# Performance work log

Measured on AMD Instinct MI355X. Metric: run time of the kernel, lower is better.

Reference implementation:

```python
import jax, jax.numpy as jnp
import numpy as np

N = 32768   # nodes
E = 524288  # edges (avg degree 16)
F = 32      # num_features
H = 512     # hidden_channels
C = 10      # num_classes
G = 64      # graphs in batch


def setup_inputs() -> dict:
    key = jax.random.key(0)
    ks = jax.random.split(key, 16)
    s = 0.05  # weight init scale
    f32 = jnp.float32
    return {
        "x": jax.random.normal(ks[0], (N, F), f32),
        "edge_index": jax.random.randint(ks[1], (2, E), 0, N),
        "batch_index": jnp.sort(jax.random.randint(ks[2], (N,), 0, G)),
        # initial_conv: F -> H  (PyG GraphConv: lin_root on x, lin_rel on aggregated neighbors)
        "w_root0": jax.random.normal(ks[3], (F, H), f32) * s,
        "w_rel0": jax.random.normal(ks[4], (F, H), f32) * s,
        "b0": jnp.zeros((H,), f32),
        # conv1..conv4 stacked: H -> H
        "w_root": jax.random.normal(ks[5], (4, H, H), f32) * s,
        "w_rel": jax.random.normal(ks[6], (4, H, H), f32) * s,
        "b": jnp.zeros((4, H), f32),
        # MLP tail
        "lin1_w": jax.random.normal(ks[7], (2 * H, H), f32) * s,
        "lin1_b": jnp.zeros((H,), f32),
        "lin2_w": jax.random.normal(ks[8], (H, H), f32) * s,
        "lin2_b": jnp.zeros((H,), f32),
        "lin3_w": jax.random.normal(ks[9], (H, C), f32) * s,
        "lin3_b": jnp.zeros((C,), f32),
    }


def _graph_conv(h, src, dst, w_root, w_rel, bias):
    # out_i = h_i @ W_root + (sum_{j->i} h_j) @ W_rel + b   (PyG GraphConv, aggr='add')
    agg = jax.ops.segment_sum(h[src], dst, num_segments=N)
    return h @ w_root + agg @ w_rel + bias


def reference(x, edge_index, batch_index,
              w_root0, w_rel0, b0, w_root, w_rel, b,
              lin1_w, lin1_b, lin2_w, lin2_b, lin3_w, lin3_b):
    src, dst = edge_index[0], edge_index[1]
    h = jnp.tanh(_graph_conv(x, src, dst, w_root0, w_rel0, b0))
    for i in range(4):  # fixed small layer loop
        h = jnp.tanh(_graph_conv(h, src, dst, w_root[i], w_rel[i], b[i]))
    # global max + mean pool over graphs
    gmax = jax.ops.segment_max(h, batch_index, num_segments=G)
    gsum = jax.ops.segment_sum(h, batch_index, num_segments=G)
    cnt = jax.ops.segment_sum(jnp.ones((N,), h.dtype), batch_index, num_segments=G)
    gmean = gsum / jnp.maximum(cnt, 1.0)[:, None]
    g = jnp.concatenate([gmax, gmean], axis=1)  # [G, 2H]
    # dropout is identity at inference (training=False)
    g = jnp.tanh(g @ lin1_w + lin1_b)
    g = jnp.tanh(g @ lin2_w + lin2_b)
    logits = g @ lin3_w + lin3_b
    return jax.nn.log_softmax(logits, axis=1)
```

## Files before the change

### kernel.cpp

```cpp
#include <hip/hip_runtime.h>
#include <hip/hip_bf16.h>
#include <math.h>

#define NN 32768
#define EE 524288
#define FF 32
#define HH 512
#define GG 64
#define CC 10

typedef __attribute__((ext_vector_type(8))) short short8;
typedef __attribute__((ext_vector_type(4))) float floatx4;

__device__ __forceinline__ float bf16_to_f32(unsigned short u) {
    union { unsigned int u; float f; } v;
    v.u = ((unsigned int)u) << 16;
    return v.f;
}
__device__ __forceinline__ unsigned short f32_to_bf16(float f) {
    union { float f; unsigned int u; } v;
    v.f = f;
    unsigned int u = v.u;
    u += 0x7FFFu + ((u >> 16) & 1u);
    return (unsigned short)(u >> 16);
}
__device__ __forceinline__ float fast_tanh(float x) {
    float e = __expf(2.0f * x);
    return 1.0f - 2.0f * __builtin_amdgcn_rcpf(e + 1.0f);
}

__global__ void prep_wt0_kernel(const float* __restrict__ wr, const float* __restrict__ wl,
                                unsigned short* __restrict__ WT0) {
    int t = blockIdx.x * blockDim.x + threadIdx.x;
    if (t >= 512 * 64) return;
    int n = t >> 6, k = t & 63;
    float v = (k < 32) ? wr[k * 512 + n] : wl[(k - 32) * 512 + n];
    WT0[t] = f32_to_bf16(v);
}

__global__ void prep_wt_kernel(const float* __restrict__ wroot, const float* __restrict__ wrel,
                               unsigned short* __restrict__ WT) {
    int t = blockIdx.x * blockDim.x + threadIdx.x;
    int l = t >> 19;
    int r = t & 524287;
    int n = r >> 10, k = r & 1023;
    float v = (k < 512) ? wroot[(size_t)l * 262144 + k * 512 + n]
                        : wrel[(size_t)l * 262144 + (k - 512) * 512 + n];
    WT[t] = f32_to_bf16(v);
}

__global__ void build_x0_kernel(const float* __restrict__ x, unsigned short* __restrict__ X0) {
    int t = blockIdx.x * blockDim.x + threadIdx.x;
    if (t >= NN * 32) return;
    int i = t >> 5, c = t & 31;
    X0[(size_t)i * 64 + c] = f32_to_bf16(x[t]);
}

__global__ void zero_i32(int* __restrict__ p, int n) {
    int i = blockIdx.x * blockDim.x + threadIdx.x;
    if (i < n) p[i] = 0;
}
__global__ void hist_kernel(const int* __restrict__ dst, int* __restrict__ counts) {
    int e = blockIdx.x * blockDim.x + threadIdx.x;
    if (e < EE) atomicAdd(&counts[dst[e]], 1);
}
__global__ __launch_bounds__(1024) void scan_kernel(const int* __restrict__ counts,
                                                    int* __restrict__ rowStart,
                                                    int* __restrict__ cursor) {
    __shared__ int part[1024];
    const int t = threadIdx.x;
    const int base = t * 32;
    int local[32];
    const int4* cp = (const int4*)(counts + base);
    int s = 0;
#pragma unroll
    for (int ii = 0; ii < 8; ++ii) {
        int4 v = cp[ii];
        local[ii * 4 + 0] = v.x; local[ii * 4 + 1] = v.y;
        local[ii * 4 + 2] = v.z; local[ii * 4 + 3] = v.w;
        s += v.x + v.y + v.z + v.w;
    }
    part[t] = s;
    __syncthreads();
    for (int off = 1; off < 1024; off <<= 1) {
        int v = (t >= off) ? part[t - off] : 0;
        __syncthreads();
        part[t] += v;
        __syncthreads();
    }
    int run = part[t] - s;
#pragma unroll
    for (int i = 0; i < 32; ++i) {
        rowStart[base + i] = run;
        cursor[base + i] = run;
        run += local[i];
    }
    if (t == 1023) rowStart[NN] = run;
}
__global__ void scatter_kernel(const int* __restrict__ src, const int* __restrict__ dst,
                               int* __restrict__ cursor, int* __restrict__ ssrc) {
    int e = blockIdx.x * blockDim.x + threadIdx.x;
    if (e < EE) {
        int p = atomicAdd(&cursor[dst[e]], 1);
        ssrc[p] = src[e];
    }
}

__device__ __forceinline__ void acc8(float* a, uint4 d) {
    a[0] += bf16_to_f32((unsigned short)(d.x & 0xFFFFu));
    a[1] += bf16_to_f32((unsigned short)(d.x >> 16));
    a[2] += bf16_to_f32((unsigned short)(d.y & 0xFFFFu));
    a[3] += bf16_to_f32((unsigned short)(d.y >> 16));
    a[4] += bf16_to_f32((unsigned short)(d.z & 0xFFFFu));
    a[5] += bf16_to_f32((unsigned short)(d.z >> 16));
    a[6] += bf16_to_f32((unsigned short)(d.w & 0xFFFFu));
    a[7] += bf16_to_f32((unsigned short)(d.w >> 16));
}

__global__ __launch_bounds__(256) void agg_kernel(const unsigned short* __restrict__ Xh, int ldh,
                                                  int cols, unsigned short* __restrict__ Xagg,
                                                  int ldagg, const int* __restrict__ rowStart,
                                                  const int* __restrict__ ssrc) {
    const int node = blockIdx.x * 4 + (threadIdx.x >> 6);
    const int lane = threadIdx.x & 63;
    const int chunks = cols >> 3;
    if (node >= NN || lane >= chunks) return;
    const int s = rowStart[node];
    const int e = rowStart[node + 1];
    float a[8] = {0.f, 0.f, 0.f, 0.f, 0.f, 0.f, 0.f, 0.f};
    const unsigned short* base = Xh + lane * 8;
    int i = s;
    for (; i + 4 <= e; i += 4) {
        int j0 = ssrc[i], j1 = ssrc[i + 1], j2 = ssrc[i + 2], j3 = ssrc[i + 3];
        uint4 d0 = *(const uint4*)(base + (size_t)j0 * ldh);
        uint4 d1 = *(const uint4*)(base + (size_t)j1 * ldh);
        uint4 d2 = *(const uint4*)(base + (size_t)j2 * ldh);
        uint4 d3 = *(const uint4*)(base + (size_t)j3 * ldh);
        acc8(a, d0); acc8(a, d1); acc8(a, d2); acc8(a, d3);
    }
    for (; i < e; ++i) {
        int j = ssrc[i];
        uint4 d = *(const uint4*)(base + (size_t)j * ldh);
        acc8(a, d);
    }
    unsigned short* out = Xagg + (size_t)node * ldagg + lane * 8;
#pragma unroll
    for (int c = 0; c < 8; ++c) out[c] = f32_to_bf16(a[c]);
}

__global__ __launch_bounds__(256) void agg_slice_kernel(const unsigned short* __restrict__ Xh,
                                                        unsigned short* __restrict__ Xagg,
                                                        const int* __restrict__ rowStart,
                                                        const int* __restrict__ ssrc) {
    const int slice = blockIdx.x & 7;
    const int nb = blockIdx.x >> 3;
    const int wv = threadIdx.x >> 6;
    const int lane = threadIdx.x & 63;
    const int ln = lane >> 3;
    const int lc = lane & 7;
    const int node = nb * 32 + wv * 8 + ln;
    const int colOff = slice * 64 + lc * 8;
    const int s = rowStart[node];
    const int e = rowStart[node + 1];
    float a[8] = {0.f, 0.f, 0.f, 0.f, 0.f, 0.f, 0.f, 0.f};
    const unsigned short* base = Xh + colOff;
    int i = s;
    for (; i + 4 <= e; i += 4) {
        int j0 = ssrc[i], j1 = ssrc[i + 1], j2 = ssrc[i + 2], j3 = ssrc[i + 3];
        uint4 d0 = *(const uint4*)(base + (size_t)j0 * 1024);
        uint4 d1 = *(const uint4*)(base + (size_t)j1 * 1024);
        uint4 d2 = *(const uint4*)(base + (size_t)j2 * 1024);
        uint4 d3 = *(const uint4*)(base + (size_t)j3 * 1024);
        acc8(a, d0); acc8(a, d1); acc8(a, d2); acc8(a, d3);
    }
    for (; i < e; ++i) {
        int j = ssrc[i];
        uint4 d = *(const uint4*)(base + (size_t)j * 1024);
        acc8(a, d);
    }
    unsigned short* out = Xagg + (size_t)node * 1024 + colOff;
#pragma unroll
    for (int c = 0; c < 8; ++c) out[c] = f32_to_bf16(a[c]);
}

__global__ __launch_bounds__(256) void gemm_bias_tanh(const unsigned short* __restrict__ Xin,
                                                      int ldin, int K,
                                                      const unsigned short* __restrict__ WT,
                                                      const float* __restrict__ bias,
                                                      unsigned short* __restrict__ Xout,
                                                      int ldout) {
    __shared__ __align__(16) unsigned short As[128 * 32];
    __shared__ __align__(16) unsigned short Bs[128 * 32];
    const int tid = threadIdx.x;
    const int lane = tid & 63;
    const int wave = tid >> 6;
    const int wm = wave >> 1, wn = wave & 1;
    const int bm = blockIdx.x, bn = blockIdx.y;

    floatx4 acc[4][4] = {};

    const int lrow = lane >> 2;
    const int lcol = (lane & 3) << 3;
    const unsigned short* Abase = Xin + (size_t)(bm * 128) * ldin;
    const unsigned short* Bbase = WT + (size_t)(bn * 128) * K;
    const int m = lane & 15;
    const int quad = lane >> 4;

    for (int k0 = 0; k0 < K; k0 += 32) {
        __syncthreads();
#pragma unroll
        for (int q = 0; q < 2; ++q) {
            const int rr = wave * 32 + q * 16;
            const unsigned short* sa = Abase + (size_t)(rr + lrow) * ldin + (k0 + lcol);
            const unsigned short* sb = Bbase + (size_t)(rr + lrow) * K + (k0 + lcol);
            __builtin_amdgcn_global_load_lds(
                (const __attribute__((address_space(1))) void*)sa,
                (__attribute__((address_space(3))) void*)(&As[rr * 32]), 16, 0, 0);
            __builtin_amdgcn_global_load_lds(
                (const __attribute__((address_space(1))) void*)sb,
                (__attribute__((address_space(3))) void*)(&Bs[rr * 32]), 16, 0, 0);
        }
        __syncthreads();
        short8 af[4], bfr[4];
#pragma unroll
        for (int t = 0; t < 4; ++t)
            af[t] = *(const short8*)&As[(wm * 64 + t * 16 + m) * 32 + quad * 8];
#pragma unroll
        for (int t = 0; t < 4; ++t)
            bfr[t] = *(const short8*)&Bs[(wn * 64 + t * 16 + m) * 32 + quad * 8];
#pragma unroll
        for (int mt = 0; mt < 4; ++mt)
#pragma unroll
            for (int nt = 0; nt < 4; ++nt)
                acc[mt][nt] =
                    __builtin_amdgcn_mfma_f32_16x16x32_bf16(af[mt], bfr[nt], acc[mt][nt], 0, 0, 0);
    }

    const int row0 = bm * 128 + wm * 64;
    const int col0 = bn * 128 + wn * 64;
#pragma unroll
    for (int mt = 0; mt < 4; ++mt) {
#pragma unroll
        for (int nt = 0; nt < 4; ++nt) {
            const int col = col0 + nt * 16 + m;
            const float bv = bias[col];
#pragma unroll
            for (int r = 0; r < 4; ++r) {
                const int row = row0 + mt * 16 + quad * 4 + r;
                float v = fast_tanh(acc[mt][nt][r] + bv);
                Xout[(size_t)row * ldout + col] = f32_to_bf16(v);
            }
        }
    }
}

__global__ __launch_bounds__(256) void pool_partial(const unsigned short* __restrict__ h,
                                                    const int* __restrict__ batch,
                                                    float* __restrict__ part) {
    const int gi = blockIdx.x, rs = blockIdx.y, t = threadIdx.x;
    int lo = 0, hi = NN;
    while (lo < hi) { int mid = (lo + hi) >> 1; if (batch[mid] < gi) lo = mid + 1; else hi = mid; }
    const int start = lo;
    hi = NN;
    while (lo < hi) { int mid = (lo + hi) >> 1; if (batch[mid] < gi + 1) lo = mid + 1; else hi = mid; }
    const int end = lo;
    const int len = end - start;
    const int q = (len + 3) >> 2;
    int r0 = start + rs * q;
    int r1 = r0 + q; if (r1 > end) r1 = end; if (r0 > end) r0 = end;
    float mx0 = -INFINITY, mx1 = -INFINITY, s0 = 0.f, s1 = 0.f;
    int i = r0;
    for (; i + 2 <= r1; i += 2) {
        unsigned int d0 = *(const unsigned int*)(h + (size_t)i * 1024 + t * 2);
        unsigned int d1 = *(const unsigned int*)(h + (size_t)(i + 1) * 1024 + t * 2);
        float v0 = bf16_to_f32((unsigned short)(d0 & 0xFFFFu));
        float v1 = bf16_to_f32((unsigned short)(d0 >> 16));
        float w0 = bf16_to_f32((unsigned short)(d1 & 0xFFFFu));
        float w1 = bf16_to_f32((unsigned short)(d1 >> 16));
        mx0 = fmaxf(mx0, fmaxf(v0, w0)); mx1 = fmaxf(mx1, fmaxf(v1, w1));
        s0 += v0 + w0; s1 += v1 + w1;
    }
    for (; i < r1; ++i) {
        unsigned int d0 = *(const unsigned int*)(h + (size_t)i * 1024 + t * 2);
        float v0 = bf16_to_f32((unsigned short)(d0 & 0xFFFFu));
        float v1 = bf16_to_f32((unsigned short)(d0 >> 16));
        mx0 = fmaxf(mx0, v0); mx1 = fmaxf(mx1, v1);
        s0 += v0; s1 += v1;
    }
    float* p = part + ((size_t)gi * 4 + rs) * 1024;
    p[t * 2] = mx0; p[t * 2 + 1] = mx1;
    p[512 + t * 2] = s0; p[512 + t * 2 + 1] = s1;
}

__global__ __launch_bounds__(256) void pool_combine(const float* __restrict__ part,
                                                    const int* __restrict__ batch,
                                                    float* __restrict__ gT) {
    const int gi = blockIdx.x, t = threadIdx.x;
    int lo = 0, hi = NN;
    while (lo < hi) { int mid = (lo + hi) >> 1; if (batch[mid] < gi) lo = mid + 1; else hi = mid; }
    const int start = lo;
    hi = NN;
    while (lo < hi) { int mid = (lo + hi) >> 1; if (batch[mid] < gi + 1) lo = mid + 1; else hi = mid; }
    int cnt = lo - start; if (cnt < 1) cnt = 1;
    const float inv = 1.0f / (float)cnt;
    float mx0 = -INFINITY, mx1 = -INFINITY, s0 = 0.f, s1 = 0.f;
#pragma unroll
    for (int rs = 0; rs < 4; ++rs) {
        const float* p = part + ((size_t)gi * 4 + rs) * 1024;
        mx0 = fmaxf(mx0, p[t * 2]); mx1 = fmaxf(mx1, p[t * 2 + 1]);
        s0 += p[512 + t * 2]; s1 += p[512 + t * 2 + 1];
    }
    gT[(size_t)(2 * t) * 64 + gi]        = mx0;
    gT[(size_t)(2 * t + 1) * 64 + gi]    = mx1;
    gT[(size_t)(512 + 2 * t) * 64 + gi]  = s0 * inv;
    gT[(size_t)(512 + 2 * t + 1) * 64 + gi] = s1 * inv;
}

__global__ __launch_bounds__(256) void mlp_splitk(const float* __restrict__ ginT,
                                                  const float* __restrict__ W,
                                                  int Ndim,
                                                  float* __restrict__ partial) {
    __shared__ float gsT[64][68];
    __shared__ float Ws[64][68];
    const int t = threadIdx.x;
    const int wv = t >> 6, l = t & 63;
    const int nb = blockIdx.x, kb = blockIdx.y;
    const int n0 = nb * 64;
    const int gr = t >> 2;
    const int c4 = (t & 3) * 16;
    float acc[16] = {};
#pragma unroll
    for (int sub = 0; sub < 2; ++sub) {
        const int k0 = kb * 128 + sub * 64;
        __syncthreads();
        {
            const float4* gsrc = (const float4*)(ginT + (size_t)(k0 + gr) * 64 + c4);
            float4* gd = (float4*)&gsT[gr][c4];
            gd[0] = gsrc[0]; gd[1] = gsrc[1]; gd[2] = gsrc[2]; gd[3] = gsrc[3];
            const float4* wsrc = (const float4*)(W + (size_t)(k0 + gr) * Ndim + n0 + c4);
            float4* wd = (float4*)&Ws[gr][c4];
            wd[0] = wsrc[0]; wd[1] = wsrc[1]; wd[2] = wsrc[2]; wd[3] = wsrc[3];
        }
        __syncthreads();
#pragma unroll 4
        for (int kk = 0; kk < 64; ++kk) {
            const float wval = Ws[kk][l];
            const float4* gv = (const float4*)&gsT[kk][wv * 16];
            float4 g0 = gv[0], g1 = gv[1], g2 = gv[2], g3 = gv[3];
            acc[0]  = fmaf(g0.x, wval, acc[0]);  acc[1]  = fmaf(g0.y, wval, acc[1]);
            acc[2]  = fmaf(g0.z, wval, acc[2]);  acc[3]  = fmaf(g0.w, wval, acc[3]);
            acc[4]  = fmaf(g1.x, wval, acc[4]);  acc[5]  = fmaf(g1.y, wval, acc[5]);
            acc[6]  = fmaf(g1.z, wval, acc[6]);  acc[7]  = fmaf(g1.w, wval, acc[7]);
            acc[8]  = fmaf(g2.x, wval, acc[8]);  acc[9]  = fmaf(g2.y, wval, acc[9]);
            acc[10] = fmaf(g2.z, wval, acc[10]); acc[11] = fmaf(g2.w, wval, acc[11]);
            acc[12] = fmaf(g3.x, wval, acc[12]); acc[13] = fmaf(g3.y, wval, acc[13]);
            acc[14] = fmaf(g3.z, wval, acc[14]); acc[15] = fmaf(g3.w, wval, acc[15]);
        }
    }
    float* p = partial + ((size_t)kb * 64) * Ndim;
#pragma unroll
    for (int g = 0; g < 16; ++g)
        p[(size_t)(wv * 16 + g) * Ndim + n0 + l] = acc[g];
}

__global__ __launch_bounds__(256) void mlp_combine(const float* __restrict__ partial, int nparts,
                                                   const float* __restrict__ bias, int Ndim,
                                                   float* __restrict__ outN,
                                                   float* __restrict__ outT) {
    const int idx = blockIdx.x * 256 + threadIdx.x;
    if (idx >= 64 * Ndim) return;
    const int g = idx / Ndim, n = idx - g * Ndim;
    float s = bias[n];
    for (int kb = 0; kb < nparts; ++kb)
        s += partial[((size_t)kb * 64 + g) * Ndim + n];
    const float v = fast_tanh(s);
    if (outN) outN[(size_t)g * Ndim + n] = v;
    if (outT) outT[(size_t)n * 64 + g] = v;
}

__global__ __launch_bounds__(64) void head_kernel(const float* __restrict__ g2,
                                                  const float* __restrict__ W,
                                                  const float* __restrict__ b,
                                                  float* __restrict__ out) {
    const int gi = blockIdx.x, t = threadIdx.x;
    const float4* gp = (const float4*)(g2 + (size_t)gi * HH + t * 8);
    float4 ga = gp[0], gb = gp[1];
    float gv[8] = {ga.x, ga.y, ga.z, ga.w, gb.x, gb.y, gb.z, gb.w};
    float logits[CC];
#pragma unroll
    for (int c = 0; c < CC; ++c) {
        float p = 0.f;
#pragma unroll
        for (int j = 0; j < 8; ++j)
            p = fmaf(gv[j], W[(t * 8 + j) * CC + c], p);
#pragma unroll
        for (int off = 32; off > 0; off >>= 1)
            p += __shfl_xor(p, off, 64);
        logits[c] = p + b[c];
    }
    if (t == 0) {
        float mx = logits[0];
#pragma unroll
        for (int c = 1; c < CC; ++c) mx = fmaxf(mx, logits[c]);
        float s = 0.f;
#pragma unroll
        for (int c = 0; c < CC; ++c) s += expf(logits[c] - mx);
        float lse = mx + logf(s);
#pragma unroll
        for (int c = 0; c < CC; ++c) out[(size_t)gi * CC + c] = logits[c] - lse;
    }
}

extern "C" void kernel_launch(void* const* d_in, const int* in_sizes, int n_in,
                              void* d_out, int out_size, void* d_ws, size_t ws_size,
                              hipStream_t stream) {
    const float* x       = (const float*)d_in[0];
    const int*   ei      = (const int*)d_in[1];
    const int*   batch   = (const int*)d_in[2];
    const float* w_root0 = (const float*)d_in[3];
    const float* w_rel0  = (const float*)d_in[4];
    const float* b0      = (const float*)d_in[5];
    const float* w_root  = (const float*)d_in[6];
    const float* w_rel   = (const float*)d_in[7];
    const float* bvec    = (const float*)d_in[8];
    const float* lin1_w  = (const float*)d_in[9];
    const float* lin1_b  = (const float*)d_in[10];
    const float* lin2_w  = (const float*)d_in[11];
    const float* lin2_b  = (const float*)d_in[12];
    const float* lin3_w  = (const float*)d_in[13];
    const float* lin3_b  = (const float*)d_in[14];
    float* out = (float*)d_out;

    char* w = (char*)d_ws;
    size_t off = 0;
    auto alloc = [&](size_t bytes) -> char* {
        char* p = w + off;
        off += (bytes + 255) & ~(size_t)255;
        return p;
    };
    unsigned short* Xa  = (unsigned short*)alloc((size_t)NN * 1024 * 2);
    unsigned short* Xb  = (unsigned short*)alloc((size_t)NN * 1024 * 2);
    unsigned short* X0  = (unsigned short*)alloc((size_t)NN * 64 * 2);
    unsigned short* WT0 = (unsigned short*)alloc(512 * 64 * 2);
    unsigned short* WTs = (unsigned short*)alloc((size_t)4 * 512 * 1024 * 2);
    int* counts   = (int*)alloc((size_t)NN * 4);
    int* rowStart = (int*)alloc((size_t)(NN + 1) * 4);
    int* cursor   = (int*)alloc((size_t)NN * 4);
    int* ssrc     = (int*)alloc((size_t)EE * 4);
    float* gbufT  = (float*)alloc((size_t)1024 * 64 * 4);
    float* g1T    = (float*)alloc((size_t)512 * 64 * 4);
    float* g2buf  = (float*)alloc((size_t)GG * 512 * 4);
    float* mlpPart = (float*)alloc((size_t)8 * 64 * 512 * 4);
    float* part   = (float*)X0;

    const int* esrc = ei;
    const int* edst = ei + EE;

    prep_wt0_kernel<<<128, 256, 0, stream>>>(w_root0, w_rel0, WT0);
    prep_wt_kernel<<<8192, 256, 0, stream>>>(w_root, w_rel, WTs);
    build_x0_kernel<<<4096, 256, 0, stream>>>(x, X0);

    zero_i32<<<128, 256, 0, stream>>>(counts, NN);
    hist_kernel<<<2048, 256, 0, stream>>>(edst, counts);
    scan_kernel<<<1, 1024, 0, stream>>>(counts, rowStart, cursor);
    scatter_kernel<<<2048, 256, 0, stream>>>(esrc, edst, cursor, ssrc);

    agg_kernel<<<8192, 256, 0, stream>>>(X0, 64, 32, X0 + 32, 64, rowStart, ssrc);
    gemm_bias_tanh<<<dim3(256, 4), 256, 0, stream>>>(X0, 64, 64, WT0, b0, Xa, 1024);

    agg_slice_kernel<<<8192, 256, 0, stream>>>(Xa, Xa + 512, rowStart, ssrc);
    gemm_bias_tanh<<<dim3(256, 4), 256, 0, stream>>>(Xa, 1024, 1024, WTs + 0 * 524288, bvec + 0, Xb, 1024);
    agg_slice_kernel<<<8192, 256, 0, stream>>>(Xb, Xb + 512, rowStart, ssrc);
    gemm_bias_tanh<<<dim3(256, 4), 256, 0, stream>>>(Xb, 1024, 1024, WTs + 1 * 524288, bvec + 512, Xa, 1024);
    agg_slice_kernel<<<8192, 256, 0, stream>>>(Xa, Xa + 512, rowStart, ssrc);
    gemm_bias_tanh<<<dim3(256, 4), 256, 0, stream>>>(Xa, 1024, 1024, WTs + 2 * 524288, bvec + 1024, Xb, 1024);
    agg_slice_kernel<<<8192, 256, 0, stream>>>(Xb, Xb + 512, rowStart, ssrc);
    gemm_bias_tanh<<<dim3(256, 4), 256, 0, stream>>>(Xb, 1024, 1024, WTs + 3 * 524288, bvec + 1536, Xa, 1024);

    pool_partial<<<dim3(GG, 4), 256, 0, stream>>>(Xa, batch, part);
    pool_combine<<<GG, 256, 0, stream>>>(part, batch, gbufT);
    mlp_splitk<<<dim3(8, 8), 256, 0, stream>>>(gbufT, lin1_w, 512, mlpPart);
    mlp_combine<<<128, 256, 0, stream>>>(mlpPart, 8, lin1_b, 512, nullptr, g1T);
    mlp_splitk<<<dim3(8, 4), 256, 0, stream>>>(g1T, lin2_w, 512, mlpPart);
    mlp_combine<<<128, 256, 0, stream>>>(mlpPart, 4, lin2_b, 512, g2buf, nullptr);
    head_kernel<<<GG, 64, 0, stream>>>(g2buf, lin3_w, lin3_b, out);
}
```

Before: 698.5 us.

## Widen GEMM K-tile with swizzled LDS, unroll gather, fuse prep kernels, split pooling

The GEMM now stages 64-wide K tiles per barrier pair, using an XOR-swizzled LDS layout, and runs two MFMA sub-steps per tile. Loading more K per tile halves the number of barriers, and the swizzle is meant to reduce LDS bank conflicts. The neighbour gather loop is unrolled to eight loads in flight, and the three preprocessing kernels are merged into one launch. Global pooling is split 16 ways per graph instead of 4 for more parallelism. In exchange, the GEMM uses more LDS per block, and the larger partial-pool buffer exactly fills the reused X0 allocation.

```diff
diff --git a/kernel.cpp b/kernel.cpp
--- a/kernel.cpp
+++ b/kernel.cpp
@@ -29,31 +29,30 @@
     return 1.0f - 2.0f * __builtin_amdgcn_rcpf(e + 1.0f);
 }
 
-__global__ void prep_wt0_kernel(const float* __restrict__ wr, const float* __restrict__ wl,
-                                unsigned short* __restrict__ WT0) {
-    int t = blockIdx.x * blockDim.x + threadIdx.x;
-    if (t >= 512 * 64) return;
-    int n = t >> 6, k = t & 63;
-    float v = (k < 32) ? wr[k * 512 + n] : wl[(k - 32) * 512 + n];
-    WT0[t] = f32_to_bf16(v);
-}
-
-__global__ void prep_wt_kernel(const float* __restrict__ wroot, const float* __restrict__ wrel,
-                               unsigned short* __restrict__ WT) {
-    int t = blockIdx.x * blockDim.x + threadIdx.x;
-    int l = t >> 19;
-    int r = t & 524287;
-    int n = r >> 10, k = r & 1023;
-    float v = (k < 512) ? wroot[(size_t)l * 262144 + k * 512 + n]
-                        : wrel[(size_t)l * 262144 + (k - 512) * 512 + n];
-    WT[t] = f32_to_bf16(v);
-}
-
-__global__ void build_x0_kernel(const float* __restrict__ x, unsigned short* __restrict__ X0) {
-    int t = blockIdx.x * blockDim.x + threadIdx.x;
-    if (t >= NN * 32) return;
-    int i = t >> 5, c = t & 31;
-    X0[(size_t)i * 64 + c] = f32_to_bf16(x[t]);
+__global__ void prep_all_kernel(const float* __restrict__ wr0, const float* __restrict__ wl0,
+                                unsigned short* __restrict__ WT0,
+                                const float* __restrict__ wroot, const float* __restrict__ wrel,
+                                unsigned short* __restrict__ WTs,
+                                const float* __restrict__ x, unsigned short* __restrict__ X0) {
+    const int b = blockIdx.x;
+    if (b < 128) {
+        int t = b * 256 + threadIdx.x;
+        int n = t >> 6, k = t & 63;
+        float v = (k < 32) ? wr0[k * 512 + n] : wl0[(k - 32) * 512 + n];
+        WT0[t] = f32_to_bf16(v);
+    } else if (b < 8320) {
+        int t = (b - 128) * 256 + threadIdx.x;
+        int l = t >> 19;
+        int r = t & 524287;
+        int n = r >> 10, k = r & 1023;
+        float v = (k < 512) ? wroot[(size_t)l * 262144 + k * 512 + n]
+                            : wrel[(size_t)l * 262144 + (k - 512) * 512 + n];
+        WTs[t] = f32_to_bf16(v);
+    } else {
+        int t = (b - 8320) * 256 + threadIdx.x;
+        int i = t >> 5, c = t & 31;
+        X0[(size_t)i * 64 + c] = f32_to_bf16(x[t]);
+    }
 }
 
 __global__ void zero_i32(int* __restrict__ p, int n) {
@@ -165,13 +164,19 @@
     float a[8] = {0.f, 0.f, 0.f, 0.f, 0.f, 0.f, 0.f, 0.f};
     const unsigned short* base = Xh + colOff;
     int i = s;
-    for (; i + 4 <= e; i += 4) {
+    for (; i + 8 <= e; i += 8) {
         int j0 = ssrc[i], j1 = ssrc[i + 1], j2 = ssrc[i + 2], j3 = ssrc[i + 3];
+        int j4 = ssrc[i + 4], j5 = ssrc[i + 5], j6 = ssrc[i + 6], j7 = ssrc[i + 7];
         uint4 d0 = *(const uint4*)(base + (size_t)j0 * 1024);
         uint4 d1 = *(const uint4*)(base + (size_t)j1 * 1024);
         uint4 d2 = *(const uint4*)(base + (size_t)j2 * 1024);
         uint4 d3 = *(const uint4*)(base + (size_t)j3 * 1024);
+        uint4 d4 = *(const uint4*)(base + (size_t)j4 * 1024);
+        uint4 d5 = *(const uint4*)(base + (size_t)j5 * 1024);
+        uint4 d6 = *(const uint4*)(base + (size_t)j6 * 1024);
+        uint4 d7 = *(const uint4*)(base + (size_t)j7 * 1024);
         acc8(a, d0); acc8(a, d1); acc8(a, d2); acc8(a, d3);
+        acc8(a, d4); acc8(a, d5); acc8(a, d6); acc8(a, d7);
     }
     for (; i < e; ++i) {
         int j = ssrc[i];
@@ -183,14 +188,14 @@
     for (int c = 0; c < 8; ++c) out[c] = f32_to_bf16(a[c]);
 }
 
-__global__ __launch_bounds__(256) void gemm_bias_tanh(const unsigned short* __restrict__ Xin,
-                                                      int ldin, int K,
-                                                      const unsigned short* __restrict__ WT,
-                                                      const float* __restrict__ bias,
-                                                      unsigned short* __restrict__ Xout,
-                                                      int ldout) {
-    __shared__ __align__(16) unsigned short As[128 * 32];
-    __shared__ __align__(16) unsigned short Bs[128 * 32];
+__global__ __launch_bounds__(256, 4) void gemm_bias_tanh(const unsigned short* __restrict__ Xin,
+                                                         int ldin, int K,
+                                                         const unsigned short* __restrict__ WT,
+                                                         const float* __restrict__ bias,
+                                                         unsigned short* __restrict__ Xout,
+                                                         int ldout) {
+    __shared__ __align__(16) unsigned short As[128 * 64];
+    __shared__ __align__(16) unsigned short Bs[128 * 64];
     const int tid = threadIdx.x;
     const int lane = tid & 63;
     const int wave = tid >> 6;
@@ -199,41 +204,51 @@
 
     floatx4 acc[4][4] = {};
 
-    const int lrow = lane >> 2;
-    const int lcol = (lane & 3) << 3;
+    const int lrow = lane >> 3;
+    const int schunk = (lane & 7) ^ (lrow & 7);
     const unsigned short* Abase = Xin + (size_t)(bm * 128) * ldin;
     const unsigned short* Bbase = WT + (size_t)(bn * 128) * K;
     const int m = lane & 15;
     const int quad = lane >> 4;
 
-    for (int k0 = 0; k0 < K; k0 += 32) {
-        __syncthreads();
-#pragma unroll
-        for (int q = 0; q < 2; ++q) {
-            const int rr = wave * 32 + q * 16;
-            const unsigned short* sa = Abase + (size_t)(rr + lrow) * ldin + (k0 + lcol);
-            const unsigned short* sb = Bbase + (size_t)(rr + lrow) * K + (k0 + lcol);
+    for (int k0 = 0; k0 < K; k0 += 64) {
+        __syncthreads();
+#pragma unroll
+        for (int q = 0; q < 4; ++q) {
+            const int rr = q * 32 + wave * 8;
+            const int row = rr + lrow;
+            const unsigned short* sa = Abase + (size_t)row * ldin + (k0 + schunk * 8);
+            const unsigned short* sb = Bbase + (size_t)row * K + (k0 + schunk * 8);
             __builtin_amdgcn_global_load_lds(
                 (const __attribute__((address_space(1))) void*)sa,
-                (__attribute__((address_space(3))) void*)(&As[rr * 32]), 16, 0, 0);
+                (__attribute__((address_space(3))) void*)(&As[rr * 64]), 16, 0, 0);
             __builtin_amdgcn_global_load_lds(
                 (const __attribute__((address_space(1))) void*)sb,
-                (__attribute__((address_space(3))) void*)(&Bs[rr * 32]), 16, 0, 0);
+                (__attribute__((address_space(3))) void*)(&Bs[rr * 64]), 16, 0, 0);
         }
         __syncthreads();
-        short8 af[4], bfr[4];
-#pragma unroll
-        for (int t = 0; t < 4; ++t)
-            af[t] = *(const short8*)&As[(wm * 64 + t * 16 + m) * 32 + quad * 8];
-#pragma unroll
-        for (int t = 0; t < 4; ++t)
-            bfr[t] = *(const short8*)&Bs[(wn * 64 + t * 16 + m) * 32 + quad * 8];
-#pragma unroll
-        for (int mt = 0; mt < 4; ++mt)
-#pragma unroll
-            for (int nt = 0; nt < 4; ++nt)
-                acc[mt][nt] =
-                    __builtin_amdgcn_mfma_f32_16x16x32_bf16(af[mt], bfr[nt], acc[mt][nt], 0, 0, 0);
+#pragma unroll
+        for (int half = 0; half < 2; ++half) {
+            short8 af[4], bfr[4];
+#pragma unroll
+            for (int t = 0; t < 4; ++t) {
+                const int row = wm * 64 + t * 16 + m;
+                const int chunk = (half * 4 + quad) ^ (row & 7);
+                af[t] = *(const short8*)&As[row * 64 + chunk * 8];
+            }
+#pragma unroll
+            for (int t = 0; t < 4; ++t) {
+                const int row = wn * 64 + t * 16 + m;
+                const int chunk = (half * 4 + quad) ^ (row & 7);
+                bfr[t] = *(const short8*)&Bs[row * 64 + chunk * 8];
+            }
+#pragma unroll
+            for (int mt = 0; mt < 4; ++mt)
+#pragma unroll
+                for (int nt = 0; nt < 4; ++nt)
+                    acc[mt][nt] = __builtin_amdgcn_mfma_f32_16x16x32_bf16(af[mt], bfr[nt],
+                                                                          acc[mt][nt], 0, 0, 0);
+        }
     }
 
     const int row0 = bm * 128 + wm * 64;
@@ -265,7 +280,7 @@
     while (lo < hi) { int mid = (lo + hi) >> 1; if (batch[mid] < gi + 1) lo = mid + 1; else hi = mid; }
     const int end = lo;
     const int len = end - start;
-    const int q = (len + 3) >> 2;
+    const int q = (len + 15) >> 4;
     int r0 = start + rs * q;
     int r1 = r0 + q; if (r1 > end) r1 = end; if (r0 > end) r0 = end;
     float mx0 = -INFINITY, mx1 = -INFINITY, s0 = 0.f, s1 = 0.f;
@@ -287,7 +302,7 @@
         mx0 = fmaxf(mx0, v0); mx1 = fmaxf(mx1, v1);
         s0 += v0; s1 += v1;
     }
-    float* p = part + ((size_t)gi * 4 + rs) * 1024;
+    float* p = part + ((size_t)gi * 16 + rs) * 1024;
     p[t * 2] = mx0; p[t * 2 + 1] = mx1;
     p[512 + t * 2] = s0; p[512 + t * 2 + 1] = s1;
 }
@@ -305,8 +320,8 @@
     const float inv = 1.0f / (float)cnt;
     float mx0 = -INFINITY, mx1 = -INFINITY, s0 = 0.f, s1 = 0.f;
 #pragma unroll
-    for (int rs = 0; rs < 4; ++rs) {
-        const float* p = part + ((size_t)gi * 4 + rs) * 1024;
+    for (int rs = 0; rs < 16; ++rs) {
+        const float* p = part + ((size_t)gi * 16 + rs) * 1024;
         mx0 = fmaxf(mx0, p[t * 2]); mx1 = fmaxf(mx1, p[t * 2 + 1]);
         s0 += p[512 + t * 2]; s1 += p[512 + t * 2 + 1];
     }
@@ -456,10 +471,7 @@
     const int* esrc = ei;
     const int* edst = ei + EE;
 
-    prep_wt0_kernel<<<128, 256, 0, stream>>>(w_root0, w_rel0, WT0);
-    prep_wt_kernel<<<8192, 256, 0, stream>>>(w_root, w_rel, WTs);
-    build_x0_kernel<<<4096, 256, 0, stream>>>(x, X0);
-
+    prep_all_kernel<<<12416, 256, 0, stream>>>(w_root0, w_rel0, WT0, w_root, w_rel, WTs, x, X0);
     zero_i32<<<128, 256, 0, stream>>>(counts, NN);
     hist_kernel<<<2048, 256, 0, stream>>>(edst, counts);
     scan_kernel<<<1, 1024, 0, stream>>>(counts, rowStart, cursor);
@@ -477,7 +489,7 @@
     agg_slice_kernel<<<8192, 256, 0, stream>>>(Xb, Xb + 512, rowStart, ssrc);
     gemm_bias_tanh<<<dim3(256, 4), 256, 0, stream>>>(Xb, 1024, 1024, WTs + 3 * 524288, bvec + 1536, Xa, 1024);
 
-    pool_partial<<<dim3(GG, 4), 256, 0, stream>>>(Xa, batch, part);
+    pool_partial<<<dim3(GG, 16), 256, 0, stream>>>(Xa, batch, part);
     pool_combine<<<GG, 256, 0, stream>>>(part, batch, gbufT);
     mlp_splitk<<<dim3(8, 8), 256, 0, stream>>>(gbufT, lin1_w, 512, mlpPart);
     mlp_combine<<<128, 256, 0, stream>>>(mlpPart, 8, lin1_b, 512, nullptr, g1T);
```

Result: faster. 668.4 us (-4.3%).
